# Performance work log

Hardware: AMD Instinct MI355X
Metric: run time of the kernel (lower is better)

The kernel has to match this reference:

```python
import jax, jax.numpy as jnp
import numpy as np

EMBED_DIM = 256
NUM_HEADS = 8
HEAD_DIM = EMBED_DIM // NUM_HEADS
SCALE = HEAD_DIM ** -0.5  # note: scale uses head_dim even though attention is over full D
EPS = 1e-12  # torch F.normalize eps


def setup_inputs() -> dict:
    key = jax.random.key(0)
    k1, k2, k3 = jax.random.split(key, 3)
    B, Nq, Nk, D = 4, 4096, 4096, EMBED_DIM
    return {
        "query": jax.random.normal(k1, (B, Nq, D), dtype=jnp.float32),
        "key": jax.random.normal(k2, (B, Nk, D), dtype=jnp.float32),
        "value": jax.random.normal(k3, (B, Nk, D), dtype=jnp.float32),
    }


def _l2_normalize(x):
    # matches torch.nn.functional.normalize(x, dim=-1): x / max(||x||, eps)
    n = jnp.linalg.norm(x, axis=-1, keepdims=True)
    return x / jnp.maximum(n, EPS)


def reference(query, key, value):
    q = _l2_normalize(query)          # (B, Nq, D)
    k = _l2_normalize(key)            # (B, Nk, D)
    scores = jnp.einsum("bqd,bkd->bqk", q, k) * SCALE  # (B, Nq, Nk) cosine sims
    attn = jax.nn.softmax(scores, axis=-1)
    return jnp.einsum("bqk,bkd->bqd", attn, value)     # (B, Nq, D)
```

## Files before the change

### kernel.cpp

```cpp
#include <hip/hip_runtime.h>


#define NQ 4096
#define DIM 256
#define NROWS 16384
#define BM 64
#define BN 64
#define KSPLIT 2
#define NITER 32
#define PSTRIDE 68

typedef __attribute__((ext_vector_type(8))) short bf16x8;
typedef __attribute__((ext_vector_type(4))) float f32x4;
typedef __attribute__((ext_vector_type(16))) float f32x16;

__device__ __forceinline__ unsigned short f2bf(float f) {
  unsigned int u = __float_as_uint(f);
  u += 0x7fffu + ((u >> 16) & 1u);
  return (unsigned short)(u >> 16);
}

__device__ __forceinline__ float bf2f(unsigned short h) {
  return __uint_as_float((unsigned int)h << 16);
}

__device__ __forceinline__ unsigned int pack2bf(float a, float b) {
  unsigned int ua = __float_as_uint(a) + 0x8000u;
  unsigned int ub = __float_as_uint(b) + 0x8000u;
  return __builtin_amdgcn_perm(ub, ua, 0x07060302u);
}

__device__ __forceinline__ void gload16(const void* g, void* l) {
  __builtin_amdgcn_global_load_lds(
      (const __attribute__((address_space(1))) unsigned int*)g,
      (__attribute__((address_space(3))) unsigned int*)l, 16, 0, 0);
}

__global__ __launch_bounds__(256) void prep(
    const float* __restrict__ K, const float* __restrict__ V,
    unsigned short* __restrict__ Kfm, unsigned short* __restrict__ Vfm)
{
  __shared__ unsigned short vt[32 * 264];
  const int blk = blockIdx.x, tid = threadIdx.x;
  const int wave = tid >> 6, lane = tid & 63;
  if (blk < 512) {
    const int kt2 = blk;
    const int kt = kt2 >> 1, h = kt2 & 1;
    #pragma unroll
    for (int i = 0; i < 8; i++) {
      const int r = wave*8 + i;
      float4 v = *(const float4*)(K + ((size_t)kt2*32 + r) * DIM + lane * 4);
      float ss = v.x*v.x + v.y*v.y + v.z*v.z + v.w*v.w;
      #pragma unroll
      for (int off = 1; off < 64; off <<= 1) ss += __shfl_xor(ss, off, 64);
      float scale = 1.0f / fmaxf(sqrtf(ss), 1e-12f);
      ushort4 o;
      o.x = f2bf(v.x*scale); o.y = f2bf(v.y*scale);
      o.z = f2bf(v.z*scale); o.w = f2bf(v.w*scale);
      *(ushort4*)(vt + r*264 + lane*4) = o;
    }
    __syncthreads();
    #pragma unroll
    for (int s = 0; s < 4; s++) {
      const int ch = tid + 256*s;
      const int c = ch >> 5, r = ch & 31;
      const int n = h*32 + r;
      bf16x8 val = *(const bf16x8*)(vt + r*264 + c*8);
      *(bf16x8*)(Kfm + (size_t)kt*16384 + (size_t)(c*64 + n)*8) = val;
    }
  } else {
    const int NS = blk - 512;
    #pragma unroll
    for (int i = 0; i < 4; i++) {
      const int e = tid + 256*i;
      const int nl = e >> 6, d = (e & 63) * 4;
      float4 v = *(const float4*)(V + ((size_t)NS*16 + nl)*DIM + d);
      ushort4 o;
      o.x = f2bf(v.x); o.y = f2bf(v.y); o.z = f2bf(v.z); o.w = f2bf(v.w);
      *(ushort4*)(vt + nl*264 + d) = o;
    }
    __syncthreads();
    #pragma unroll
    for (int i = 0; i < 2; i++) {
      const int ch = tid + 256*i;
      const int db = ch >> 6, ln = ch & 63;
      const int row0 = (ln >> 5) * 8, dd = db*32 + (ln & 31);
      ushort4 a, b;
      a.x = vt[(row0+0)*264 + dd]; a.y = vt[(row0+1)*264 + dd];
      a.z = vt[(row0+2)*264 + dd]; a.w = vt[(row0+3)*264 + dd];
      b.x = vt[(row0+4)*264 + dd]; b.y = vt[(row0+5)*264 + dd];
      b.z = vt[(row0+6)*264 + dd]; b.w = vt[(row0+7)*264 + dd];
      size_t base = ((size_t)(NS*8 + db)*64 + ln)*8;
      *(ushort4*)(Vfm + base)     = a;
      *(ushort4*)(Vfm + base + 4) = b;
    }
  }
}

__global__ __launch_bounds__(512, 4) void attn(
    const float* __restrict__ Qg,
    const unsigned short* __restrict__ Kfm,
    const unsigned short* __restrict__ Vfm,
    unsigned short* __restrict__ Opart, float* __restrict__ lpart)
{
  __shared__ unsigned short Klds[32 * 64 * 8];
  __shared__ unsigned short Plds[BM * PSTRIDE];

  const int tid = threadIdx.x, wave = tid >> 6, lane = tid & 63;
  const int l15 = lane & 15, l4 = lane >> 4;
  const int blk = blockIdx.x;
  const int g = blk & 7, qt = blk >> 3;
  const int b = g >> 1, ks = g & 1;
  const int Rq0 = b*NQ + qt*BM;
  const int n0base = b*NQ + ks*(NQ/KSPLIT);
  const int mi = wave & 1, ni = wave >> 1;

  {
    unsigned short* Qlds = Klds;
    #pragma unroll
    for (int i = 0; i < 8; i++) {
      const int r = wave*8 + i;
      float4 v = *(const float4*)(Qg + (size_t)(Rq0 + r)*DIM + lane*4);
      float ss = v.x*v.x + v.y*v.y + v.z*v.z + v.w*v.w;
      #pragma unroll
      for (int off = 1; off < 64; off <<= 1) ss += __shfl_xor(ss, off, 64);
      float scale = (0.17677669529663687f * 1.4426950408889634f)
                    / fmaxf(sqrtf(ss), 1e-12f);
      ushort4 o;
      o.x = f2bf(v.x*scale); o.y = f2bf(v.y*scale);
      o.z = f2bf(v.z*scale); o.w = f2bf(v.w*scale);
      *(ushort4*)(Qlds + r*DIM + lane*4) = o;
    }
  }
  __syncthreads();

  bf16x8 qf[2][8];
  #pragma unroll
  for (int mt = 0; mt < 2; mt++) {
    const unsigned short* qrow = Klds + (mi*32 + mt*16 + l15)*DIM + l4*8;
    #pragma unroll
    for (int kg = 0; kg < 8; kg++)
      qf[mt][kg] = *(const bf16x8*)(qrow + kg*32);
  }
  __syncthreads();

  f32x16 oacc[2] = {};
  float lacc[2] = {};

  auto stage = [&](int kt_) {
    const unsigned short* src = Kfm + (size_t)((n0base + kt_*BN) >> 6) * (32*64*8);
    #pragma unroll
    for (int jj = 0; jj < 4; jj++) {
      const int c = wave*4 + jj;
      gload16(src + (size_t)c*512 + lane*8, Klds + (size_t)c*512);
    }
  };

  stage(0);

  for (int kt = 0; kt < NITER; kt++) {
    __syncthreads();

    f32x4 sacc[2] = {};
    #pragma unroll
    for (int kg = 0; kg < 8; kg++) {
      const int nrow = ni*16 + l15;
      const int c = kg*4 + l4;
      bf16x8 kf = *(const bf16x8*)(Klds + ((size_t)(c*64 + nrow))*8);
      __builtin_amdgcn_s_setprio(1);
      #pragma unroll
      for (int mt = 0; mt < 2; mt++)
        sacc[mt] = __builtin_amdgcn_mfma_f32_16x16x32_bf16(
            kf, qf[mt][kg], sacc[mt], 0, 0, 0);
      __builtin_amdgcn_s_setprio(0);
    }

    #pragma unroll
    for (int mt = 0; mt < 2; mt++) {
      float p0 = __builtin_amdgcn_exp2f(sacc[mt][0]);
      float p1 = __builtin_amdgcn_exp2f(sacc[mt][1]);
      float p2 = __builtin_amdgcn_exp2f(sacc[mt][2]);
      float p3 = __builtin_amdgcn_exp2f(sacc[mt][3]);
      lacc[mt] += (p0 + p1) + (p2 + p3);
      uint2 pk;
      pk.x = pack2bf(p0, p1);
      pk.y = pack2bf(p2, p3);
      const int m = mi*32 + mt*16 + l15;
      const int n = ni*16 + 4*l4;
      *(uint2*)(Plds + m*PSTRIDE + n) = pk;
    }

    __syncthreads();

    if (kt + 1 < NITER) stage(kt + 1);

    const int NB0 = (n0base + kt*BN) >> 4;
    #pragma unroll
    for (int kstep = 0; kstep < 4; kstep++) {
      bf16x8 pf[2], vf;
      #pragma unroll
      for (int mt2 = 0; mt2 < 2; mt2++)
        pf[mt2] = *(const bf16x8*)(Plds + (mt2*32 + (lane & 31))*PSTRIDE
                                   + kstep*16 + 8*(lane >> 5));
      vf = *(const bf16x8*)(Vfm + ((size_t)((NB0 + kstep)*8 + wave)*64 + lane)*8);
      __builtin_amdgcn_s_setprio(1);
      #pragma unroll
      for (int mt2 = 0; mt2 < 2; mt2++)
        oacc[mt2] = __builtin_amdgcn_mfma_f32_32x32x16_bf16(
            pf[mt2], vf, oacc[mt2], 0, 0, 0);
      __builtin_amdgcn_s_setprio(0);
    }
  }

  #pragma unroll
  for (int mt = 0; mt < 2; mt++) {
    float s = lacc[mt];
    s += __shfl_xor(s, 16, 64);
    s += __shfl_xor(s, 32, 64);
    if (l4 == 0)
      lpart[(size_t)(ks*4 + ni)*NROWS + Rq0 + mi*32 + mt*16 + l15] = s;
  }

  const int d = wave*32 + (lane & 31);
  #pragma unroll
  for (int mt2 = 0; mt2 < 2; mt2++)
    #pragma unroll
    for (int reg = 0; reg < 16; reg++) {
      const int m = mt2*32 + 4*(lane >> 5) + (reg & 3) + 8*(reg >> 2);
      Opart[((size_t)(ks*NROWS + Rq0 + m))*DIM + d] = f2bf(oacc[mt2][reg]);
    }
}

__global__ __launch_bounds__(256) void combine(
    const unsigned short* __restrict__ Opart, const float* __restrict__ lpart,
    float* __restrict__ out)
{
  const size_t idx = (size_t)blockIdx.x*256 + threadIdx.x;
  const size_t e = idx*4;
  const int R = (int)(e >> 8);
  float ls = 0.0f;
  #pragma unroll
  for (int i = 0; i < 8; i++) ls += lpart[(size_t)i*NROWS + R];
  float inv = 1.0f / ls;
  ushort4 o0 = *(const ushort4*)(Opart + e);
  ushort4 o1 = *(const ushort4*)(Opart + (size_t)NROWS*DIM + e);
  float4 o;
  o.x = (bf2f(o0.x) + bf2f(o1.x))*inv;
  o.y = (bf2f(o0.y) + bf2f(o1.y))*inv;
  o.z = (bf2f(o0.z) + bf2f(o1.z))*inv;
  o.w = (bf2f(o0.w) + bf2f(o1.w))*inv;
  *(float4*)(out + e) = o;
}

extern "C" void kernel_launch(void* const* d_in, const int* in_sizes, int n_in,
                              void* d_out, int out_size, void* d_ws, size_t ws_size,
                              hipStream_t stream) {
  const float* Q = (const float*)d_in[0];
  const float* K = (const float*)d_in[1];
  const float* V = (const float*)d_in[2];
  char* ws = (char*)d_ws;
  unsigned short* Kfm   = (unsigned short*)(ws);
  unsigned short* Vfm   = (unsigned short*)(ws + 8388608);
  unsigned short* Opart = (unsigned short*)(ws + 16777216);
  float* lpart = (float*)(ws + 33554432);

  prep<<<1536, 256, 0, stream>>>(K, V, Kfm, Vfm);
  attn<<<512, 512, 0, stream>>>(Q, Kfm, Vfm, Opart, lpart);
  combine<<<4096, 256, 0, stream>>>(Opart, lpart, (float*)d_out);
}
```

Baseline: 194.2 us.

## Keep P in registers via permlane swap and restructure attention tiling

Restructures the attention kernel: 4 waves of 256 threads, each owning 32 query rows and computing the full 256-wide output. Query tiles grow to 128 rows, key tiles shrink to 32, and the key dimension is split four ways. Scores use 32x32 MFMAs whose output is converted to the PV A-operand layout in registers with cvt_pk_bf16 and permlane32_swap, so the P round trip through shared memory and one barrier per iteration go away. K tiles are double buffered in LDS and Q is normalized straight into registers. In exchange, per-thread register pressure rises (8 f32x16 accumulators), partial-output traffic doubles with KSPLIT=4, and the combine kernel now reads four partials.

New measurement: 221.0 us. +13.8%, slower.

```diff
diff --git a/kernel.cpp b/kernel.cpp
--- a/kernel.cpp
+++ b/kernel.cpp
@@ -4,14 +4,12 @@
 #define NQ 4096
 #define DIM 256
 #define NROWS 16384
-#define BM 64
-#define BN 64
-#define KSPLIT 2
+#define BM 128
+#define BN 32
+#define KSPLIT 4
 #define NITER 32
-#define PSTRIDE 68
 
 typedef __attribute__((ext_vector_type(8))) short bf16x8;
-typedef __attribute__((ext_vector_type(4))) float f32x4;
 typedef __attribute__((ext_vector_type(16))) float f32x16;
 
 __device__ __forceinline__ unsigned short f2bf(float f) {
@@ -22,12 +20,6 @@
 
 __device__ __forceinline__ float bf2f(unsigned short h) {
   return __uint_as_float((unsigned int)h << 16);
-}
-
-__device__ __forceinline__ unsigned int pack2bf(float a, float b) {
-  unsigned int ua = __float_as_uint(a) + 0x8000u;
-  unsigned int ub = __float_as_uint(b) + 0x8000u;
-  return __builtin_amdgcn_perm(ub, ua, 0x07060302u);
 }
 
 __device__ __forceinline__ void gload16(const void* g, void* l) {
@@ -44,12 +36,11 @@
   const int blk = blockIdx.x, tid = threadIdx.x;
   const int wave = tid >> 6, lane = tid & 63;
   if (blk < 512) {
-    const int kt2 = blk;
-    const int kt = kt2 >> 1, h = kt2 & 1;
+    const int kt = blk;
     #pragma unroll
     for (int i = 0; i < 8; i++) {
       const int r = wave*8 + i;
-      float4 v = *(const float4*)(K + ((size_t)kt2*32 + r) * DIM + lane * 4);
+      float4 v = *(const float4*)(K + ((size_t)kt*32 + r) * DIM + lane * 4);
       float ss = v.x*v.x + v.y*v.y + v.z*v.z + v.w*v.w;
       #pragma unroll
       for (int off = 1; off < 64; off <<= 1) ss += __shfl_xor(ss, off, 64);
@@ -64,9 +55,8 @@
     for (int s = 0; s < 4; s++) {
       const int ch = tid + 256*s;
       const int c = ch >> 5, r = ch & 31;
-      const int n = h*32 + r;
       bf16x8 val = *(const bf16x8*)(vt + r*264 + c*8);
-      *(bf16x8*)(Kfm + (size_t)kt*16384 + (size_t)(c*64 + n)*8) = val;
+      *(bf16x8*)(Kfm + (size_t)kt*8192 + c*256 + r*8) = val;
     }
   } else {
     const int NS = blk - 512;
@@ -97,137 +87,125 @@
   }
 }
 
-__global__ __launch_bounds__(512, 4) void attn(
+__global__ __launch_bounds__(256, 2) void attn(
     const float* __restrict__ Qg,
     const unsigned short* __restrict__ Kfm,
     const unsigned short* __restrict__ Vfm,
     unsigned short* __restrict__ Opart, float* __restrict__ lpart)
 {
-  __shared__ unsigned short Klds[32 * 64 * 8];
-  __shared__ unsigned short Plds[BM * PSTRIDE];
+  __shared__ unsigned short Klds[2][BN * DIM];
 
   const int tid = threadIdx.x, wave = tid >> 6, lane = tid & 63;
-  const int l15 = lane & 15, l4 = lane >> 4;
+  const int l31 = lane & 31, hi = lane >> 5;
   const int blk = blockIdx.x;
-  const int g = blk & 7, qt = blk >> 3;
-  const int b = g >> 1, ks = g & 1;
+  const int g = blk & 15, qt = blk >> 4;
+  const int b = g >> 2, ks = g & 3;
   const int Rq0 = b*NQ + qt*BM;
-  const int n0base = b*NQ + ks*(NQ/KSPLIT);
-  const int mi = wave & 1, ni = wave >> 1;
-
+  const int n0 = b*NQ + ks*(NQ/KSPLIT);
+  const int m0 = Rq0 + wave*32 + l31;
+
+  bf16x8 qf[16];
   {
-    unsigned short* Qlds = Klds;
-    #pragma unroll
-    for (int i = 0; i < 8; i++) {
-      const int r = wave*8 + i;
-      float4 v = *(const float4*)(Qg + (size_t)(Rq0 + r)*DIM + lane*4);
-      float ss = v.x*v.x + v.y*v.y + v.z*v.z + v.w*v.w;
-      #pragma unroll
-      for (int off = 1; off < 64; off <<= 1) ss += __shfl_xor(ss, off, 64);
-      float scale = (0.17677669529663687f * 1.4426950408889634f)
-                    / fmaxf(sqrtf(ss), 1e-12f);
-      ushort4 o;
-      o.x = f2bf(v.x*scale); o.y = f2bf(v.y*scale);
-      o.z = f2bf(v.z*scale); o.w = f2bf(v.w*scale);
-      *(ushort4*)(Qlds + r*DIM + lane*4) = o;
-    }
-  }
-  __syncthreads();
-
-  bf16x8 qf[2][8];
+    const float* qrow = Qg + (size_t)m0*DIM + hi*8;
+    float ss = 0.f;
+    #pragma unroll
+    for (int kg = 0; kg < 16; kg++) {
+      float4 a = *(const float4*)(qrow + kg*16);
+      float4 c = *(const float4*)(qrow + kg*16 + 4);
+      ss += a.x*a.x + a.y*a.y + a.z*a.z + a.w*a.w
+          + c.x*c.x + c.y*c.y + c.z*c.z + c.w*c.w;
+    }
+    ss += __shfl_xor(ss, 32, 64);
+    const float scale = (0.17677669529663687f * 1.4426950408889634f)
+                        / fmaxf(sqrtf(ss), 1e-12f);
+    #pragma unroll
+    for (int kg = 0; kg < 16; kg++) {
+      float4 a = *(const float4*)(qrow + kg*16);
+      float4 c = *(const float4*)(qrow + kg*16 + 4);
+      union { unsigned short u[8]; bf16x8 v; } o;
+      o.u[0] = f2bf(a.x*scale); o.u[1] = f2bf(a.y*scale);
+      o.u[2] = f2bf(a.z*scale); o.u[3] = f2bf(a.w*scale);
+      o.u[4] = f2bf(c.x*scale); o.u[5] = f2bf(c.y*scale);
+      o.u[6] = f2bf(c.z*scale); o.u[7] = f2bf(c.w*scale);
+      qf[kg] = o.v;
+    }
+  }
+
+  f32x16 oacc[8] = {};
+  float lacc = 0.f;
+
+  auto stage = [&](int t) {
+    const unsigned short* src = Kfm + ((size_t)(n0 >> 5) + t) * 8192;
+    unsigned short* dst = &Klds[t & 1][0];
+    #pragma unroll
+    for (int c = 0; c < 4; c++)
+      gload16(src + (wave*4 + c)*512 + lane*8, dst + (wave*4 + c)*512);
+  };
+
+  stage(0);
+
+  for (int t = 0; t < NITER; t++) {
+    __syncthreads();
+    if (t + 1 < NITER) stage(t + 1);
+
+    const unsigned short* kb = &Klds[t & 1][0];
+    f32x16 sa = {}, sb = {};
+    __builtin_amdgcn_s_setprio(1);
+    #pragma unroll
+    for (int kg = 0; kg < 16; kg++) {
+      bf16x8 kf = *(const bf16x8*)(kb + ((kg*2 + hi)*32 + l31)*8);
+      if (kg & 1)
+        sb = __builtin_amdgcn_mfma_f32_32x32x16_bf16(kf, qf[kg], sb, 0, 0, 0);
+      else
+        sa = __builtin_amdgcn_mfma_f32_32x32x16_bf16(kf, qf[kg], sa, 0, 0, 0);
+    }
+    __builtin_amdgcn_s_setprio(0);
+
+    float p[16];
+    #pragma unroll
+    for (int r = 0; r < 16; r++)
+      p[r] = __builtin_amdgcn_exp2f(sa[r] + sb[r]);
+    #pragma unroll
+    for (int r = 0; r < 16; r++) lacc += p[r];
+
+    auto mkfrag = [](const float* pp) -> bf16x8 {
+      unsigned int a0, a1, b0, b1;
+      asm("v_cvt_pk_bf16_f32 %0, %1, %2" : "=v"(a0) : "v"(pp[0]), "v"(pp[1]));
+      asm("v_cvt_pk_bf16_f32 %0, %1, %2" : "=v"(b0) : "v"(pp[4]), "v"(pp[5]));
+      asm("v_cvt_pk_bf16_f32 %0, %1, %2" : "=v"(a1) : "v"(pp[2]), "v"(pp[3]));
+      asm("v_cvt_pk_bf16_f32 %0, %1, %2" : "=v"(b1) : "v"(pp[6]), "v"(pp[7]));
+      asm volatile("v_permlane32_swap_b32 %0, %1" : "+v"(a0), "+v"(b0));
+      asm volatile("v_permlane32_swap_b32 %0, %1" : "+v"(a1), "+v"(b1));
+      union { unsigned int u[4]; bf16x8 v; } r;
+      r.u[0] = a0; r.u[1] = a1; r.u[2] = b0; r.u[3] = b1;
+      return r.v;
+    };
+    const bf16x8 pa0 = mkfrag(p);
+    const bf16x8 pa1 = mkfrag(p + 8);
+
+    const int nb = (n0 + t*BN) >> 4;
+    #pragma unroll
+    for (int db = 0; db < 8; db++) {
+      bf16x8 v0 = *(const bf16x8*)(Vfm + ((size_t)((nb  )*8 + db)*64 + lane)*8);
+      bf16x8 v1 = *(const bf16x8*)(Vfm + ((size_t)((nb+1)*8 + db)*64 + lane)*8);
+      __builtin_amdgcn_s_setprio(1);
+      oacc[db] = __builtin_amdgcn_mfma_f32_32x32x16_bf16(pa0, v0, oacc[db], 0, 0, 0);
+      oacc[db] = __builtin_amdgcn_mfma_f32_32x32x16_bf16(pa1, v1, oacc[db], 0, 0, 0);
+      __builtin_amdgcn_s_setprio(0);
+    }
+  }
+
+  lacc += __shfl_xor(lacc, 32, 64);
+  if (hi == 0)
+    lpart[(size_t)ks*NROWS + Rq0 + wave*32 + l31] = lacc;
+
   #pragma unroll
-  for (int mt = 0; mt < 2; mt++) {
-    const unsigned short* qrow = Klds + (mi*32 + mt*16 + l15)*DIM + l4*8;
-    #pragma unroll
-    for (int kg = 0; kg < 8; kg++)
-      qf[mt][kg] = *(const bf16x8*)(qrow + kg*32);
-  }
-  __syncthreads();
-
-  f32x16 oacc[2] = {};
-  float lacc[2] = {};
-
-  auto stage = [&](int kt_) {
-    const unsigned short* src = Kfm + (size_t)((n0base + kt_*BN) >> 6) * (32*64*8);
-    #pragma unroll
-    for (int jj = 0; jj < 4; jj++) {
-      const int c = wave*4 + jj;
-      gload16(src + (size_t)c*512 + lane*8, Klds + (size_t)c*512);
-    }
-  };
-
-  stage(0);
-
-  for (int kt = 0; kt < NITER; kt++) {
-    __syncthreads();
-
-    f32x4 sacc[2] = {};
-    #pragma unroll
-    for (int kg = 0; kg < 8; kg++) {
-      const int nrow = ni*16 + l15;
-      const int c = kg*4 + l4;
-      bf16x8 kf = *(const bf16x8*)(Klds + ((size_t)(c*64 + nrow))*8);
-      __builtin_amdgcn_s_setprio(1);
-      #pragma unroll
-      for (int mt = 0; mt < 2; mt++)
-        sacc[mt] = __builtin_amdgcn_mfma_f32_16x16x32_bf16(
-            kf, qf[mt][kg], sacc[mt], 0, 0, 0);
-      __builtin_amdgcn_s_setprio(0);
-    }
-
-    #pragma unroll
-    for (int mt = 0; mt < 2; mt++) {
-      float p0 = __builtin_amdgcn_exp2f(sacc[mt][0]);
-      float p1 = __builtin_amdgcn_exp2f(sacc[mt][1]);
-      float p2 = __builtin_amdgcn_exp2f(sacc[mt][2]);
-      float p3 = __builtin_amdgcn_exp2f(sacc[mt][3]);
-      lacc[mt] += (p0 + p1) + (p2 + p3);
-      uint2 pk;
-      pk.x = pack2bf(p0, p1);
-      pk.y = pack2bf(p2, p3);
-      const int m = mi*32 + mt*16 + l15;
-      const int n = ni*16 + 4*l4;
-      *(uint2*)(Plds + m*PSTRIDE + n) = pk;
-    }
-
-    __syncthreads();
-
-    if (kt + 1 < NITER) stage(kt + 1);
-
-    const int NB0 = (n0base + kt*BN) >> 4;
-    #pragma unroll
-    for (int kstep = 0; kstep < 4; kstep++) {
-      bf16x8 pf[2], vf;
-      #pragma unroll
-      for (int mt2 = 0; mt2 < 2; mt2++)
-        pf[mt2] = *(const bf16x8*)(Plds + (mt2*32 + (lane & 31))*PSTRIDE
-                                   + kstep*16 + 8*(lane >> 5));
-      vf = *(const bf16x8*)(Vfm + ((size_t)((NB0 + kstep)*8 + wave)*64 + lane)*8);
-      __builtin_amdgcn_s_setprio(1);
-      #pragma unroll
-      for (int mt2 = 0; mt2 < 2; mt2++)
-        oacc[mt2] = __builtin_amdgcn_mfma_f32_32x32x16_bf16(
-            pf[mt2], vf, oacc[mt2], 0, 0, 0);
-      __builtin_amdgcn_s_setprio(0);
-    }
-  }
-
-  #pragma unroll
-  for (int mt = 0; mt < 2; mt++) {
-    float s = lacc[mt];
-    s += __shfl_xor(s, 16, 64);
-    s += __shfl_xor(s, 32, 64);
-    if (l4 == 0)
-      lpart[(size_t)(ks*4 + ni)*NROWS + Rq0 + mi*32 + mt*16 + l15] = s;
-  }
-
-  const int d = wave*32 + (lane & 31);
-  #pragma unroll
-  for (int mt2 = 0; mt2 < 2; mt2++)
+  for (int db = 0; db < 8; db++)
     #pragma unroll
     for (int reg = 0; reg < 16; reg++) {
-      const int m = mt2*32 + 4*(lane >> 5) + (reg & 3) + 8*(reg >> 2);
-      Opart[((size_t)(ks*NROWS + Rq0 + m))*DIM + d] = f2bf(oacc[mt2][reg]);
+      const int m = 4*hi + (reg & 3) + 8*(reg >> 2);
+      Opart[((size_t)(ks*NROWS + Rq0 + wave*32 + m))*DIM + db*32 + l31]
+          = f2bf(oacc[db][reg]);
     }
 }
 
@@ -240,15 +218,16 @@
   const int R = (int)(e >> 8);
   float ls = 0.0f;
   #pragma unroll
-  for (int i = 0; i < 8; i++) ls += lpart[(size_t)i*NROWS + R];
+  for (int i = 0; i < 4; i++) ls += lpart[(size_t)i*NROWS + R];
   float inv = 1.0f / ls;
-  ushort4 o0 = *(const ushort4*)(Opart + e);
-  ushort4 o1 = *(const ushort4*)(Opart + (size_t)NROWS*DIM + e);
-  float4 o;
-  o.x = (bf2f(o0.x) + bf2f(o1.x))*inv;
-  o.y = (bf2f(o0.y) + bf2f(o1.y))*inv;
-  o.z = (bf2f(o0.z) + bf2f(o1.z))*inv;
-  o.w = (bf2f(o0.w) + bf2f(o1.w))*inv;
+  float4 o = {0.f, 0.f, 0.f, 0.f};
+  #pragma unroll
+  for (int s = 0; s < 4; s++) {
+    ushort4 op = *(const ushort4*)(Opart + (size_t)s*NROWS*DIM + e);
+    o.x += bf2f(op.x); o.y += bf2f(op.y);
+    o.z += bf2f(op.z); o.w += bf2f(op.w);
+  }
+  o.x *= inv; o.y *= inv; o.z *= inv; o.w *= inv;
   *(float4*)(out + e) = o;
 }
 
@@ -262,9 +241,9 @@
   unsigned short* Kfm   = (unsigned short*)(ws);
   unsigned short* Vfm   = (unsigned short*)(ws + 8388608);
   unsigned short* Opart = (unsigned short*)(ws + 16777216);
-  float* lpart = (float*)(ws + 33554432);
+  float* lpart = (float*)(ws + 16777216 + 33554432);
 
   prep<<<1536, 256, 0, stream>>>(K, V, Kfm, Vfm);
-  attn<<<512, 512, 0, stream>>>(Q, Kfm, Vfm, Opart, lpart);
+  attn<<<512, 256, 0, stream>>>(Q, Kfm, Vfm, Opart, lpart);
   combine<<<4096, 256, 0, stream>>>(Opart, lpart, (float*)d_out);
 }
```
